# Performance work log

Measured on AMD Instinct MI355X. Metric: run time of the kernel, lower is better.

The kernel has to match this reference:

```python
import jax, jax.numpy as jnp
import numpy as np

N = 10000      # nodes
E = 160000     # edges
B = 16         # graphs in batch
F_NODE = 42
F_EDGE = 12
D = 256        # hidden_dim
H = 4          # heads
C = D // H     # per-head channels = 64
L = 5          # num_layers
NEG_SLOPE = 0.2  # GATConv leaky_relu slope


def layernorm(x, g, b, eps=1e-5):
    mu = jnp.mean(x, axis=-1, keepdims=True)
    var = jnp.var(x, axis=-1, keepdims=True)
    return (x - mu) * jax.lax.rsqrt(var + eps) * g + b


def setup_inputs() -> dict:
    key = jax.random.key(0)
    ks = jax.random.split(key, 20)
    def w(i, shape, scale=0.05):
        return jax.random.normal(ks[i], shape, dtype=jnp.float32) * scale
    return {
        "x": jax.random.normal(ks[0], (N, F_NODE), dtype=jnp.float32),
        "edge_attr": jax.random.normal(ks[1], (E, F_EDGE), dtype=jnp.float32),
        "edge_index": jax.random.randint(ks[2], (2, E), 0, N),
        "batch": jnp.sort(jax.random.randint(ks[3], (N,), 0, B)),
        # node / edge encoders
        "enc_w": w(4, (F_NODE, D)), "enc_b": jnp.zeros((D,), jnp.float32),
        "eenc_w": w(5, (F_EDGE, D)), "eenc_b": jnp.zeros((D,), jnp.float32),
        # stacked GAT layer params [L, ...]
        "gat_w": w(6, (L, D, D)),          # lin_src == lin_dst (shared in PyG for Tensor input)
        "att_src": w(7, (L, H, C)),
        "att_dst": w(8, (L, H, C)),
        "att_edge": w(9, (L, H, C)),
        "gat_ew": w(10, (L, D, D)),        # lin_edge
        "gat_b": jnp.zeros((L, D), jnp.float32),
        "ln_g": jnp.ones((L, D), jnp.float32),
        "ln_b": jnp.zeros((L, D), jnp.float32),
        # attention pooling gate MLP
        "gate_w1": w(11, (D, D)), "gate_b1": jnp.zeros((D,), jnp.float32),
        "gate_w2": w(12, (D, 1)), "gate_b2": jnp.zeros((1,), jnp.float32),
        # MLP readout (mlp_layers=2)
        "ro_w1": w(13, (D, D)), "ro_b1": jnp.zeros((D,), jnp.float32),
        "ro_w2": w(14, (D, D)), "ro_b2": jnp.zeros((D,), jnp.float32),
    }


def reference(x, edge_index, edge_attr, batch, enc_w, enc_b, eenc_w, eenc_b,
              gat_w, att_src, att_dst, att_edge, gat_ew, gat_b, ln_g, ln_b,
              gate_w1, gate_b1, gate_w2, gate_b2, ro_w1, ro_b1, ro_w2, ro_b2):
    src0, dst0 = edge_index[0], edge_index[1]

    # encoders (dropout is identity at eval)
    h = jax.nn.relu(x @ enc_w + enc_b)                      # [N, D]
    e = jax.nn.relu(edge_attr @ eenc_w + eenc_b)            # [E, D]

    # GATConv add_self_loops with fill_value='mean': self-loop edge feature is
    # the mean of incoming edge features per destination node.
    esum = jax.ops.segment_sum(e, dst0, num_segments=N)
    cnt = jax.ops.segment_sum(jnp.ones((E,), e.dtype), dst0, num_segments=N)
    e_self = esum / jnp.maximum(cnt, 1.0)[:, None]
    e_full = jnp.concatenate([e, e_self], axis=0)           # [E+N, D]
    loops = jnp.arange(N)
    src = jnp.concatenate([src0, loops])
    dst = jnp.concatenate([dst0, loops])

    for l in range(L):
        xh = (h @ gat_w[l]).reshape(N, H, C)                # [N, H, C]
        a_s = jnp.einsum('nhc,hc->nh', xh, att_src[l])      # [N, H]
        a_d = jnp.einsum('nhc,hc->nh', xh, att_dst[l])
        eh = (e_full @ gat_ew[l]).reshape(-1, H, C)         # [E+N, H, C]
        a_e = jnp.einsum('ehc,hc->eh', eh, att_edge[l])
        alpha = jax.nn.leaky_relu(a_s[src] + a_d[dst] + a_e, NEG_SLOPE)  # [E+N, H]
        # softmax over incoming edges per destination node (stable)
        m = jax.lax.stop_gradient(jax.ops.segment_max(alpha, dst, num_segments=N))
        ex = jnp.exp(alpha - m[dst])
        den = jax.ops.segment_sum(ex, dst, num_segments=N)
        attn = ex / den[dst]                                # [E+N, H]
        msg = xh[src] * attn[:, :, None]                    # [E+N, H, C]
        out = jax.ops.segment_sum(msg, dst, num_segments=N).reshape(N, D) + gat_b[l]
        out = jax.nn.relu(layernorm(out, ln_g[l], ln_b[l]))
        h = h + out                                         # residual

    # GlobalAttention pooling: softmax(gate_nn(h)) per graph, weighted sum
    gate = (jax.nn.relu(h @ gate_w1 + gate_b1) @ gate_w2 + gate_b2)[:, 0]  # [N]
    gm = jax.lax.stop_gradient(jax.ops.segment_max(gate, batch, num_segments=B))
    ge = jnp.exp(gate - gm[batch])
    gd = jax.ops.segment_sum(ge, batch, num_segments=B)
    wgt = ge / gd[batch]
    g_embed = jax.ops.segment_sum(h * wgt[:, None], batch, num_segments=B)  # [B, D]

    # MLP readout
    return jax.nn.relu(g_embed @ ro_w1 + ro_b1) @ ro_w2 + ro_b2  # [B, D]
```

## Files before the change

### kernel.cpp

```cpp
#include <hip/hip_runtime.h>
#include <math.h>

#define DD 256
#define HH 4
#define CC 64
#define LL 5
#define NEG_SLOPE 0.2f
#define LH 20
#define WCAP 192

typedef __bf16 bf16x8 __attribute__((ext_vector_type(8)));
typedef __bf16 bf16x4 __attribute__((ext_vector_type(4)));
typedef float f32x4 __attribute__((ext_vector_type(4)));

static __device__ __forceinline__ float lrelu(float x) {
    return x > 0.0f ? x : NEG_SLOPE * x;
}

__global__ __launch_bounds__(256) void mega_setup_kernel(
    const float* __restrict__ gat_ew, const float* __restrict__ att_edge,
    float* __restrict__ wproj,
    const float* __restrict__ gat_w, const float* __restrict__ gate_w1,
    __bf16* __restrict__ wf,
    const int* __restrict__ dst_arr, int* __restrict__ deg,
    const float* __restrict__ x, const float* __restrict__ enc_w,
    const float* __restrict__ enc_b, float* __restrict__ h,
    __bf16* __restrict__ hbf,
    float* __restrict__ g_embed, float* __restrict__ gate_out,
    int N, int E, int B) {
    int blk = blockIdx.x;
    int tid = threadIdx.x;
    int EB = (E + 255) >> 8;
    if (blk < 5) {
        int l = blk;
        int k = tid;
        const float* W = gat_ew + (size_t)l * DD * DD;
        const float* att = att_edge + l * DD;
        for (int hh = 0; hh < HH; ++hh) {
            float s = 0.f;
            #pragma unroll
            for (int c = 0; c < CC; ++c)
                s += W[k * DD + hh * CC + c] * att[hh * CC + c];
            wproj[k * LH + l * HH + hh] = s;
        }
        return;
    }
    blk -= 5;
    if (blk < 192) {
        int b = blk;
        int l = b >> 5;
        int rem = b & 31;
        int y = rem >> 3, ks = rem & 7;
        int t = tid >> 6, lane = tid & 63;
        int q = lane >> 4, r15 = lane & 15;
        const float* W = (l < 5) ? (gat_w + (size_t)l * DD * DD) : gate_w1;
        size_t obase = (((size_t)b * 4 + t) * 64 + lane) * 8;
        int kbase = ks * 32 + q * 8;
        int col = y * 64 + t * 16 + r15;
        #pragma unroll
        for (int j = 0; j < 8; ++j)
            wf[obase + j] = (__bf16)W[(size_t)(kbase + j) * DD + col];
        return;
    }
    blk -= 192;
    if (blk < EB) {
        int e = blk * 256 + tid;
        if (e < E) atomicAdd(&deg[dst_arr[e]], 1);
        return;
    }
    blk -= EB;
    if (blk < N) {
        int n = blk;
        __shared__ float xs[42];
        if (tid < 42) xs[tid] = x[(size_t)n * 42 + tid];
        __syncthreads();
        float acc = enc_b[tid];
        #pragma unroll
        for (int f = 0; f < 42; ++f) acc += xs[f] * enc_w[f * DD + tid];
        float v = fmaxf(acc, 0.f);
        h[(size_t)n * DD + tid] = v;
        hbf[(size_t)n * DD + tid] = (__bf16)v;
        return;
    }
    blk -= N;
    if (blk == 0) {
        for (int i = tid; i < B * DD; i += 256) g_embed[i] = 0.f;
        return;
    }
    for (int i = tid; i < N; i += 256) gate_out[i] = 0.f;
}

__global__ __launch_bounds__(1024) void scan_pack_kernel(
    const int* __restrict__ deg, int* __restrict__ row_ptr,
    int* __restrict__ cursor, int n,
    const float* __restrict__ eenc_w, const float* __restrict__ eenc_b,
    const float* __restrict__ wproj, __bf16* __restrict__ wfe,
    __bf16* __restrict__ wfp) {
    int tid = threadIdx.x;
    if (blockIdx.x == 1) {
        {
            int idx = tid;
            int t = idx >> 6, lane = idx & 63;
            int q = lane >> 4, r15 = lane & 15;
            int col = t * 16 + r15;
            #pragma unroll
            for (int j = 0; j < 8; ++j) {
                int k = q * 8 + j;
                float v = (k < 12) ? eenc_w[k * 256 + col]
                                   : (k == 12 ? eenc_b[col] : 0.f);
                wfe[(size_t)idx * 8 + j] = (__bf16)v;
            }
        }
        {
            int idx = tid;
            int sidx = idx >> 6, lane = idx & 63;
            int s = sidx >> 1, t2 = sidx & 1;
            int q = lane >> 4, r15 = lane & 15;
            int col = t2 * 16 + r15;
            #pragma unroll
            for (int j = 0; j < 8; ++j) {
                int k = s * 32 + q * 8 + j;
                float v = (col < LH) ? wproj[k * LH + col] : 0.f;
                wfp[(size_t)idx * 8 + j] = (__bf16)v;
            }
        }
        return;
    }
    __shared__ int wsum[16];
    __shared__ int carry_s;
    int w = tid >> 6, lane = tid & 63;
    if (tid == 0) carry_s = 0;
    __syncthreads();
    for (int base = 0; base < n; base += 1024) {
        int i = base + tid;
        int v = (i < n) ? deg[i] : 0;
        int carry = carry_s;
        int s = v;
        #pragma unroll
        for (int off = 1; off < 64; off <<= 1) {
            int t = __shfl_up(s, off, 64);
            if (lane >= off) s += t;
        }
        if (lane == 63) wsum[w] = s;
        __syncthreads();
        if (w == 0 && lane < 16) {
            int ws = wsum[lane];
            #pragma unroll
            for (int off = 1; off < 16; off <<= 1) {
                int t = __shfl_up(ws, off, 64);
                if (lane >= off) ws += t;
            }
            wsum[lane] = ws;
        }
        __syncthreads();
        int waveoff = (w == 0) ? 0 : wsum[w - 1];
        if (i < n) {
            int ex = carry + waveoff + s - v;
            row_ptr[i] = ex;
            cursor[i] = ex;
        }
        __syncthreads();
        if (tid == 0) carry_s = carry + wsum[15];
        __syncthreads();
    }
    if (tid == 0) row_ptr[n] = carry_s;
}

__global__ void scatter_kernel(const int* __restrict__ src, const int* __restrict__ dst,
                               int* __restrict__ cursor, int* __restrict__ csr_src,
                               int* __restrict__ pos, int E) {
    int e = blockIdx.x * 256 + threadIdx.x;
    if (e >= E) return;
    int d = dst[e];
    int pk = atomicAdd(&cursor[d], 1);
    csr_src[pk] = src[e];
    pos[e] = pk;
}

__global__ __launch_bounds__(256) void edge_mfma_kernel(
    const float* __restrict__ edge_attr, const __bf16* __restrict__ wfe,
    const __bf16* __restrict__ wfp, const int* __restrict__ pos,
    float* __restrict__ a_e_csr, int E) {
    __shared__ __bf16 sm[4][16][264];
    int tid = threadIdx.x;
    int w = tid >> 6, lane = tid & 63;
    int q = lane >> 4, r15 = lane & 15;
    int eb = blockIdx.x * 64 + w * 16;
    int e = eb + r15;
    int ec = min(e, E - 1);
    bf16x8 a1;
    #pragma unroll
    for (int j = 0; j < 8; ++j) a1[j] = (__bf16)0.f;
    if (q == 0) {
        const float4* p = (const float4*)(edge_attr + (size_t)ec * 12);
        float4 p0 = p[0], p1 = p[1];
        a1[0] = (__bf16)p0.x; a1[1] = (__bf16)p0.y; a1[2] = (__bf16)p0.z; a1[3] = (__bf16)p0.w;
        a1[4] = (__bf16)p1.x; a1[5] = (__bf16)p1.y; a1[6] = (__bf16)p1.z; a1[7] = (__bf16)p1.w;
    } else if (q == 1) {
        float4 p2 = *(const float4*)(edge_attr + (size_t)ec * 12 + 8);
        a1[0] = (__bf16)p2.x; a1[1] = (__bf16)p2.y; a1[2] = (__bf16)p2.z; a1[3] = (__bf16)p2.w;
        a1[4] = (__bf16)1.0f;
    }
    const bf16x8* wfeP = (const bf16x8*)wfe;
    f32x4 zero = (f32x4){0.f, 0.f, 0.f, 0.f};
    #pragma unroll
    for (int t = 0; t < 16; ++t) {
        bf16x8 bfr = wfeP[t * 64 + lane];
        f32x4 c = __builtin_amdgcn_mfma_f32_16x16x32_bf16(a1, bfr, zero, 0, 0, 0);
        int col = t * 16 + r15;
        #pragma unroll
        for (int r = 0; r < 4; ++r)
            sm[w][q * 4 + r][col] = (__bf16)fmaxf(c[r], 0.f);
    }
    const bf16x8* wfpP = (const bf16x8*)wfp;
    f32x4 c2[2];
    c2[0] = zero; c2[1] = zero;
    #pragma unroll
    for (int s = 0; s < 8; ++s) {
        bf16x8 a2 = *(const bf16x8*)&sm[w][r15][s * 32 + q * 8];
        #pragma unroll
        for (int t2 = 0; t2 < 2; ++t2)
            c2[t2] = __builtin_amdgcn_mfma_f32_16x16x32_bf16(
                a2, wfpP[(s * 2 + t2) * 64 + lane], c2[t2], 0, 0, 0);
    }
    #pragma unroll
    for (int t2 = 0; t2 < 2; ++t2) {
        int col = t2 * 16 + r15;
        if (col >= LH) continue;
        #pragma unroll
        for (int r = 0; r < 4; ++r) {
            int e2 = eb + q * 4 + r;
            if (e2 < E) {
                int pk = pos[e2];
                a_e_csr[(size_t)pk * LH + col] = c2[t2][r];
            }
        }
    }
}

__global__ void self_ae_kernel(const int* __restrict__ row_ptr,
                               float* __restrict__ a_e_csr, int N, int E) {
    int i = blockIdx.x * 256 + threadIdx.x;
    if (i >= N * LH) return;
    int n = i / LH;
    int j = i % LH;
    int rs = row_ptr[n], re = row_ptr[n + 1];
    float s = 0.f;
    for (int k = rs; k < re; ++k)
        s += a_e_csr[(size_t)k * LH + j];
    a_e_csr[(size_t)(E + n) * LH + j] = s / (float)max(re - rs, 1);
}

__global__ __launch_bounds__(256) void gemm_mfma_kernel(
    const __bf16* __restrict__ hbf, const __bf16* __restrict__ wf,
    __bf16* __restrict__ xhbf, int M,
    const float* __restrict__ att_src, const float* __restrict__ att_dst,
    float* __restrict__ a_s, float* __restrict__ a_d,
    const float* __restrict__ bias, const float* __restrict__ gate_w2,
    const float* __restrict__ gate_b2, float* __restrict__ gate_out) {
    int tid = threadIdx.x;
    int w = tid >> 6, lane = tid & 63;
    int q = lane >> 4, r15 = lane & 15;
    int m0 = blockIdx.x * 64;
    int y2 = blockIdx.y;
    int arow = m0 + w * 16 + r15;
    int arowc = min(arow, M - 1);
    const __bf16* ap = hbf + (size_t)arowc * DD + q * 8;
    const bf16x8* wfP = (const bf16x8*)wf;
    f32x4 acc[8];
    #pragma unroll
    for (int g = 0; g < 8; ++g) acc[g] = (f32x4){0.f, 0.f, 0.f, 0.f};
    #pragma unroll
    for (int ks = 0; ks < 8; ++ks) {
        bf16x8 a = *(const bf16x8*)(ap + ks * 32);
        #pragma unroll
        for (int g = 0; g < 8; ++g) {
            int y = y2 * 2 + (g >> 2);
            int t = g & 3;
            bf16x8 b = wfP[(size_t)(((y * 8 + ks) * 4) + t) * 64 + lane];
            acc[g] = __builtin_amdgcn_mfma_f32_16x16x32_bf16(a, b, acc[g], 0, 0, 0);
        }
    }
    if (xhbf) {
        #pragma unroll
        for (int g = 0; g < 8; ++g) {
            int col = (y2 * 8 + g) * 16 + r15;
            #pragma unroll
            for (int r = 0; r < 4; ++r) {
                int rc = m0 + w * 16 + q * 4 + r;
                if (rc < M) xhbf[(size_t)rc * DD + col] = (__bf16)acc[g][r];
            }
        }
    }
    if (att_src) {
        #pragma unroll
        for (int r = 0; r < 4; ++r) {
            float ps0 = 0.f, pd0 = 0.f, ps1 = 0.f, pd1 = 0.f;
            #pragma unroll
            for (int g = 0; g < 8; ++g) {
                int col = (y2 * 8 + g) * 16 + r15;
                float v = acc[g][r];
                if (g < 4) { ps0 += v * att_src[col]; pd0 += v * att_dst[col]; }
                else       { ps1 += v * att_src[col]; pd1 += v * att_dst[col]; }
            }
            #pragma unroll
            for (int mask = 1; mask < 16; mask <<= 1) {
                ps0 += __shfl_xor(ps0, mask, 64);
                pd0 += __shfl_xor(pd0, mask, 64);
                ps1 += __shfl_xor(ps1, mask, 64);
                pd1 += __shfl_xor(pd1, mask, 64);
            }
            int rc = m0 + w * 16 + q * 4 + r;
            if (r15 == 0 && rc < M) {
                a_s[rc * HH + y2 * 2 + 0] = ps0;
                a_d[rc * HH + y2 * 2 + 0] = pd0;
                a_s[rc * HH + y2 * 2 + 1] = ps1;
                a_d[rc * HH + y2 * 2 + 1] = pd1;
            }
        }
    }
    if (gate_w2) {
        #pragma unroll
        for (int r = 0; r < 4; ++r) {
            float pg = 0.f;
            #pragma unroll
            for (int g = 0; g < 8; ++g) {
                int col = (y2 * 8 + g) * 16 + r15;
                pg += fmaxf(acc[g][r] + bias[col], 0.f) * gate_w2[col];
            }
            #pragma unroll
            for (int mask = 1; mask < 16; mask <<= 1) pg += __shfl_xor(pg, mask, 64);
            int rc = m0 + w * 16 + q * 4 + r;
            if (r15 == 0 && rc < M) {
                float add = pg + (y2 == 0 ? gate_b2[0] : 0.f);
                atomicAdd(&gate_out[rc], add);
            }
        }
    }
}

__global__ __launch_bounds__(256) void gat_message7_kernel(
    const __bf16* __restrict__ xhbf, const float* __restrict__ a_s,
    const float* __restrict__ a_d, const float* __restrict__ a_e,
    const int* __restrict__ row_ptr, const int* __restrict__ csr_src,
    const float* __restrict__ gat_b,
    const float* __restrict__ ln_g, const float* __restrict__ ln_b,
    float* __restrict__ h, __bf16* __restrict__ hbf, int N, int E) {
    __shared__ float lws[4][WCAP * 4];
    __shared__ int lsrc[4][WCAP];
    int tid = threadIdx.x;
    int w = tid >> 6, lane = tid & 63;
    int n = blockIdx.x * 4 + w;
    if (n >= N) return;
    int hh = lane >> 4, j = lane & 15;
    int rs = row_ptr[n], re = row_ptr[n + 1];
    int deg = re - rs;
    float adn = a_d[n * HH + hh];
    float al_self = lrelu(a_s[n * HH + hh] + adn + a_e[(size_t)(E + n) * LH + hh]);
    float m = al_self, den = 0.f;
    for (int k = rs + j; k < re; k += 16) {
        int kk = k - rs;
        int s = csr_src[k];
        float a = lrelu(a_s[s * HH + hh] + adn + a_e[(size_t)k * LH + hh]);
        if (kk < WCAP) {
            lws[w][kk * 4 + hh] = a;
            if (hh == 0) lsrc[w][kk] = s;
        }
        float mn = fmaxf(m, a);
        den = den * __expf(m - mn) + __expf(a - mn);
        m = mn;
    }
    #pragma unroll
    for (int off = 1; off < 16; off <<= 1) {
        float m2 = __shfl_xor(m, off, 64);
        float d2 = __shfl_xor(den, off, 64);
        float mn = fmaxf(m, m2);
        den = den * __expf(m - mn) + d2 * __expf(m2 - mn);
        m = mn;
    }
    den += __expf(al_self - m);
    float inv_den = 1.0f / den;
    int cap = min(deg, WCAP);
    for (int kk = j; kk < cap; kk += 16)
        lws[w][kk * 4 + hh] = __expf(lws[w][kk * 4 + hh] - m) * inv_den;
    float wself = __expf(al_self - m) * inv_den;
    bf16x4 xsb = *((const bf16x4*)(xhbf + (size_t)n * DD) + lane);
    float4 acc;
    acc.x = wself * (float)xsb[0]; acc.y = wself * (float)xsb[1];
    acc.z = wself * (float)xsb[2]; acc.w = wself * (float)xsb[3];
    int k = rs;
    for (; k + 1 < re; k += 2) {
        int kk0 = k - rs, kk1 = kk0 + 1;
        int s0, s1_;
        float w0, w1;
        if (kk1 < WCAP) {
            s0 = lsrc[w][kk0]; s1_ = lsrc[w][kk1];
            w0 = lws[w][kk0 * 4 + hh]; w1 = lws[w][kk1 * 4 + hh];
        } else {
            s0 = csr_src[k]; s1_ = csr_src[k + 1];
            w0 = (kk0 < WCAP) ? lws[w][kk0 * 4 + hh]
               : __expf(lrelu(a_s[s0 * HH + hh] + adn + a_e[(size_t)k * LH + hh]) - m) * inv_den;
            w1 = __expf(lrelu(a_s[s1_ * HH + hh] + adn + a_e[(size_t)(k + 1) * LH + hh]) - m) * inv_den;
        }
        bf16x4 x0 = *((const bf16x4*)(xhbf + (size_t)s0 * DD) + lane);
        bf16x4 x1 = *((const bf16x4*)(xhbf + (size_t)s1_ * DD) + lane);
        acc.x += w0 * (float)x0[0] + w1 * (float)x1[0];
        acc.y += w0 * (float)x0[1] + w1 * (float)x1[1];
        acc.z += w0 * (float)x0[2] + w1 * (float)x1[2];
        acc.w += w0 * (float)x0[3] + w1 * (float)x1[3];
    }
    if (k < re) {
        int kk0 = k - rs;
        int s0;
        float w0;
        if (kk0 < WCAP) { s0 = lsrc[w][kk0]; w0 = lws[w][kk0 * 4 + hh]; }
        else {
            s0 = csr_src[k];
            w0 = __expf(lrelu(a_s[s0 * HH + hh] + adn + a_e[(size_t)k * LH + hh]) - m) * inv_den;
        }
        bf16x4 x0 = *((const bf16x4*)(xhbf + (size_t)s0 * DD) + lane);
        acc.x += w0 * (float)x0[0]; acc.y += w0 * (float)x0[1];
        acc.z += w0 * (float)x0[2]; acc.w += w0 * (float)x0[3];
    }
    float4 gb = *((const float4*)gat_b + lane);
    float4 val;
    val.x = acc.x + gb.x; val.y = acc.y + gb.y;
    val.z = acc.z + gb.z; val.w = acc.w + gb.w;
    float s1 = val.x + val.y + val.z + val.w;
    float s2 = val.x * val.x + val.y * val.y + val.z * val.z + val.w * val.w;
    #pragma unroll
    for (int off = 1; off < 64; off <<= 1) {
        s1 += __shfl_xor(s1, off, 64);
        s2 += __shfl_xor(s2, off, 64);
    }
    float mu = s1 * (1.0f / DD);
    float var = s2 * (1.0f / DD) - mu * mu;
    float rstd = rsqrtf(var + 1e-5f);
    float4 lg = *((const float4*)ln_g + lane);
    float4 lb = *((const float4*)ln_b + lane);
    float4 nv;
    nv.x = fmaxf((val.x - mu) * rstd * lg.x + lb.x, 0.f);
    nv.y = fmaxf((val.y - mu) * rstd * lg.y + lb.y, 0.f);
    nv.z = fmaxf((val.z - mu) * rstd * lg.z + lb.z, 0.f);
    nv.w = fmaxf((val.w - mu) * rstd * lg.w + lb.w, 0.f);
    float4* hp = (float4*)(h + (size_t)n * DD) + lane;
    float4 hv = *hp;
    hv.x += nv.x; hv.y += nv.y; hv.z += nv.z; hv.w += nv.w;
    *hp = hv;
    bf16x4 hb;
    hb[0] = (__bf16)hv.x; hb[1] = (__bf16)hv.y;
    hb[2] = (__bf16)hv.z; hb[3] = (__bf16)hv.w;
    *((bf16x4*)(hbf + (size_t)n * DD) + lane) = hb;
}

__global__ __launch_bounds__(256) void gseg_kernel(
    const float* __restrict__ gate, const int* __restrict__ batch,
    float* __restrict__ gmax, float* __restrict__ gden, int N) {
    int b = blockIdx.x;
    int tid = threadIdx.x;
    __shared__ int bounds[2];
    if (tid < 2) {
        int target = b + tid;
        int lo = 0, hi = N;
        while (lo < hi) {
            int mid = (lo + hi) >> 1;
            if (batch[mid] < target) lo = mid + 1; else hi = mid;
        }
        bounds[tid] = lo;
    }
    __syncthreads();
    int s0 = bounds[0], s1 = bounds[1];
    __shared__ float red[256];
    float m = -1e30f;
    for (int i = s0 + tid; i < s1; i += 256) m = fmaxf(m, gate[i]);
    red[tid] = m;
    __syncthreads();
    for (int off = 128; off; off >>= 1) {
        if (tid < off) red[tid] = fmaxf(red[tid], red[tid + off]);
        __syncthreads();
    }
    float gm = red[0];
    __syncthreads();
    float s = 0.f;
    for (int i = s0 + tid; i < s1; i += 256) s += __expf(gate[i] - gm);
    red[tid] = s;
    __syncthreads();
    for (int off = 128; off; off >>= 1) {
        if (tid < off) red[tid] += red[tid + off];
        __syncthreads();
    }
    if (tid == 0) {
        gmax[b] = gm;
        gden[b] = red[0];
    }
}

#define POOL_CHUNK 32
__global__ __launch_bounds__(256) void pool_scatter_kernel(
    const float* __restrict__ h, const float* __restrict__ gate,
    const float* __restrict__ gmax, const float* __restrict__ gden,
    const int* __restrict__ batch, float* __restrict__ g_embed, int N) {
    int i0 = blockIdx.x * POOL_CHUNK;
    int d = threadIdx.x;
    int iend = min(i0 + POOL_CHUNK, N);
    float acc = 0.f;
    int cur = batch[i0];
    for (int i = i0; i < iend; ++i) {
        int b = batch[i];
        if (b != cur) {
            atomicAdd(&g_embed[cur * DD + d], acc);
            acc = 0.f;
            cur = b;
        }
        float wgt = __expf(gate[i] - gmax[b]) / gden[b];
        acc += wgt * h[(size_t)i * DD + d];
    }
    atomicAdd(&g_embed[cur * DD + d], acc);
}

__global__ __launch_bounds__(256) void readout_kernel(
    const float* __restrict__ g_embed, const float* __restrict__ w1,
    const float* __restrict__ b1, const float* __restrict__ w2,
    const float* __restrict__ b2, float* __restrict__ out) {
    int b = blockIdx.x;
    int tid = threadIdx.x;
    __shared__ float gvec[256];
    __shared__ float hid[256];
    gvec[tid] = g_embed[b * DD + tid];
    __syncthreads();
    float hv = b1[tid];
    for (int k = 0; k < DD; ++k) hv += gvec[k] * w1[k * DD + tid];
    hid[tid] = fmaxf(hv, 0.f);
    __syncthreads();
    float o = b2[tid];
    for (int t = 0; t < DD; ++t) o += hid[t] * w2[t * DD + tid];
    out[b * DD + tid] = o;
}

extern "C" void kernel_launch(void* const* d_in, const int* in_sizes, int n_in,
                              void* d_out, int out_size, void* d_ws, size_t ws_size,
                              hipStream_t stream) {
    const float* x        = (const float*)d_in[0];
    const float* edge_attr= (const float*)d_in[1];
    const int*   edge_idx = (const int*)d_in[2];
    const int*   batch    = (const int*)d_in[3];
    const float* enc_w    = (const float*)d_in[4];
    const float* enc_b    = (const float*)d_in[5];
    const float* eenc_w   = (const float*)d_in[6];
    const float* eenc_b   = (const float*)d_in[7];
    const float* gat_w    = (const float*)d_in[8];
    const float* att_src  = (const float*)d_in[9];
    const float* att_dst  = (const float*)d_in[10];
    const float* att_edge = (const float*)d_in[11];
    const float* gat_ew   = (const float*)d_in[12];
    const float* gat_b    = (const float*)d_in[13];
    const float* ln_g     = (const float*)d_in[14];
    const float* ln_b     = (const float*)d_in[15];
    const float* gate_w1  = (const float*)d_in[16];
    const float* gate_b1  = (const float*)d_in[17];
    const float* gate_w2  = (const float*)d_in[18];
    const float* gate_b2  = (const float*)d_in[19];
    const float* ro_w1    = (const float*)d_in[20];
    const float* ro_b1    = (const float*)d_in[21];
    const float* ro_w2    = (const float*)d_in[22];
    const float* ro_b2    = (const float*)d_in[23];
    float* out = (float*)d_out;

    const int N = in_sizes[0] / 42;
    const int E = in_sizes[1] / 12;
    const int B = out_size / DD;

    char* p = (char*)d_ws;
    auto alloc = [&](size_t bytes) {
        char* r = p;
        p += (bytes + 255) & ~(size_t)255;
        return (void*)r;
    };
    float*  h       = (float*)alloc((size_t)N * DD * 4);
    __bf16* hbf     = (__bf16*)alloc((size_t)N * DD * 2);
    __bf16* xhbf    = (__bf16*)alloc((size_t)N * DD * 2);
    float*  a_s     = (float*)alloc((size_t)N * HH * 4);
    float*  a_d     = (float*)alloc((size_t)N * HH * 4);
    float*  a_e_csr = (float*)alloc((size_t)(E + N) * LH * 4);
    float*  wproj   = (float*)alloc((size_t)DD * LH * 4);
    __bf16* wfe     = (__bf16*)alloc((size_t)16 * 64 * 8 * 2);
    __bf16* wfp     = (__bf16*)alloc((size_t)16 * 64 * 8 * 2);
    __bf16* wf      = (__bf16*)alloc((size_t)6 * DD * DD * 2);
    float*  gate    = (float*)alloc((size_t)N * 4);
    float*  g_embed = (float*)alloc((size_t)B * DD * 4);
    float*  gmax    = (float*)alloc((size_t)B * 4);
    float*  gden    = (float*)alloc((size_t)B * 4);
    int* deg        = (int*)alloc((size_t)N * 4);
    int* row_ptr    = (int*)alloc((size_t)(N + 1) * 4);
    int* cursor     = (int*)alloc((size_t)N * 4);
    int* csr_src    = (int*)alloc((size_t)E * 4);
    int* pos        = (int*)alloc((size_t)E * 4);

    const int* src_arr = edge_idx;
    const int* dst_arr = edge_idx + E;

    hipMemsetAsync(deg, 0, (size_t)N * 4, stream);

    const int EB = (E + 255) / 256;
    int mega_grid = 5 + 192 + EB + N + 2;
    mega_setup_kernel<<<mega_grid, 256, 0, stream>>>(
        gat_ew, att_edge, wproj, gat_w, gate_w1, wf,
        dst_arr, deg, x, enc_w, enc_b, h, hbf, g_embed, gate, N, E, B);
    scan_pack_kernel<<<2, 1024, 0, stream>>>(
        deg, row_ptr, cursor, N, eenc_w, eenc_b, wproj, wfe, wfp);
    scatter_kernel<<<(E + 255) / 256, 256, 0, stream>>>(
        src_arr, dst_arr, cursor, csr_src, pos, E);
    edge_mfma_kernel<<<(E + 63) / 64, 256, 0, stream>>>(
        edge_attr, wfe, wfp, pos, a_e_csr, E);
    self_ae_kernel<<<(N * LH + 255) / 256, 256, 0, stream>>>(
        row_ptr, a_e_csr, N, E);

    dim3 ggrid((N + 63) / 64, 2);
    for (int l = 0; l < LL; ++l) {
        gemm_mfma_kernel<<<ggrid, 256, 0, stream>>>(
            hbf, wf + (size_t)l * DD * DD, xhbf, N,
            att_src + l * DD, att_dst + l * DD, a_s, a_d,
            nullptr, nullptr, nullptr, nullptr);
        gat_message7_kernel<<<(N + 3) / 4, 256, 0, stream>>>(
            xhbf, a_s, a_d, a_e_csr + l * HH, row_ptr, csr_src,
            gat_b + l * DD, ln_g + l * DD, ln_b + l * DD, h, hbf, N, E);
    }

    gemm_mfma_kernel<<<ggrid, 256, 0, stream>>>(
        hbf, wf + (size_t)5 * DD * DD, nullptr, N,
        nullptr, nullptr, nullptr, nullptr,
        gate_b1, gate_w2, gate_b2, gate);
    gseg_kernel<<<B, 256, 0, stream>>>(gate, batch, gmax, gden, N);
    pool_scatter_kernel<<<(N + POOL_CHUNK - 1) / POOL_CHUNK, 256, 0, stream>>>(
        h, gate, gmax, gden, batch, g_embed, N);
    readout_kernel<<<B, 256, 0, stream>>>(g_embed, ro_w1, ro_b1, ro_w2, ro_b2, out);
}
```

Before: 402.6 us.

## Fuse CSR scatter into edge MFMA, split edge attention per layer, unroll gather by four

Removes the separate scatter kernel by doing the atomic cursor slot assignment and csr_src write inside the edge MFMA kernel, keeping slot indices in shared memory instead of a pos array. The edge attention logits move from an interleaved [E+N, 20] layout to per-layer [L][E+N][4] planes, so each message-passing layer reads a contiguous 16-byte row per edge instead of striding over 80 bytes. The message aggregation loop gains a fast path for degree at most WCAP that unrolls the neighbor gather by four, putting more loads in flight. The fusion adds atomics into the MFMA kernel.

```diff
diff --git a/kernel.cpp b/kernel.cpp
--- a/kernel.cpp
+++ b/kernel.cpp
@@ -166,28 +166,26 @@
     if (tid == 0) row_ptr[n] = carry_s;
 }
 
-__global__ void scatter_kernel(const int* __restrict__ src, const int* __restrict__ dst,
-                               int* __restrict__ cursor, int* __restrict__ csr_src,
-                               int* __restrict__ pos, int E) {
-    int e = blockIdx.x * 256 + threadIdx.x;
-    if (e >= E) return;
-    int d = dst[e];
-    int pk = atomicAdd(&cursor[d], 1);
-    csr_src[pk] = src[e];
-    pos[e] = pk;
-}
-
 __global__ __launch_bounds__(256) void edge_mfma_kernel(
     const float* __restrict__ edge_attr, const __bf16* __restrict__ wfe,
-    const __bf16* __restrict__ wfp, const int* __restrict__ pos,
-    float* __restrict__ a_e_csr, int E) {
+    const __bf16* __restrict__ wfp,
+    const int* __restrict__ src_arr, const int* __restrict__ dst_arr,
+    int* __restrict__ cursor, int* __restrict__ csr_src,
+    float* __restrict__ a_e, int E, int N) {
     __shared__ __bf16 sm[4][16][264];
+    __shared__ int pkbuf[4][16];
     int tid = threadIdx.x;
     int w = tid >> 6, lane = tid & 63;
     int q = lane >> 4, r15 = lane & 15;
     int eb = blockIdx.x * 64 + w * 16;
     int e = eb + r15;
     int ec = min(e, E - 1);
+    if (q == 0 && e < E) {
+        int d = dst_arr[e];
+        int pk = atomicAdd(&cursor[d], 1);
+        csr_src[pk] = src_arr[e];
+        pkbuf[w][r15] = pk;
+    }
     bf16x8 a1;
     #pragma unroll
     for (int j = 0; j < 8; ++j) a1[j] = (__bf16)0.f;
@@ -223,32 +221,36 @@
             c2[t2] = __builtin_amdgcn_mfma_f32_16x16x32_bf16(
                 a2, wfpP[(s * 2 + t2) * 64 + lane], c2[t2], 0, 0, 0);
     }
+    size_t stride_l = (size_t)(E + N) * 4;
     #pragma unroll
     for (int t2 = 0; t2 < 2; ++t2) {
         int col = t2 * 16 + r15;
         if (col >= LH) continue;
+        int l = col >> 2, hh = col & 3;
         #pragma unroll
         for (int r = 0; r < 4; ++r) {
             int e2 = eb + q * 4 + r;
             if (e2 < E) {
-                int pk = pos[e2];
-                a_e_csr[(size_t)pk * LH + col] = c2[t2][r];
+                int pk = pkbuf[w][q * 4 + r];
+                a_e[(size_t)l * stride_l + (size_t)pk * 4 + hh] = c2[t2][r];
             }
         }
     }
 }
 
 __global__ void self_ae_kernel(const int* __restrict__ row_ptr,
-                               float* __restrict__ a_e_csr, int N, int E) {
+                               float* __restrict__ a_e, int N, int E) {
     int i = blockIdx.x * 256 + threadIdx.x;
     if (i >= N * LH) return;
     int n = i / LH;
     int j = i % LH;
+    int l = j >> 2, hh = j & 3;
     int rs = row_ptr[n], re = row_ptr[n + 1];
+    size_t base = (size_t)l * (size_t)(E + N) * 4;
     float s = 0.f;
     for (int k = rs; k < re; ++k)
-        s += a_e_csr[(size_t)k * LH + j];
-    a_e_csr[(size_t)(E + n) * LH + j] = s / (float)max(re - rs, 1);
+        s += a_e[base + (size_t)k * 4 + hh];
+    a_e[base + (size_t)(E + n) * 4 + hh] = s / (float)max(re - rs, 1);
 }
 
 __global__ __launch_bounds__(256) void gemm_mfma_kernel(
@@ -339,7 +341,7 @@
     }
 }
 
-__global__ __launch_bounds__(256) void gat_message7_kernel(
+__global__ __launch_bounds__(256) void gat_message8_kernel(
     const __bf16* __restrict__ xhbf, const float* __restrict__ a_s,
     const float* __restrict__ a_d, const float* __restrict__ a_e,
     const int* __restrict__ row_ptr, const int* __restrict__ csr_src,
@@ -356,12 +358,12 @@
     int rs = row_ptr[n], re = row_ptr[n + 1];
     int deg = re - rs;
     float adn = a_d[n * HH + hh];
-    float al_self = lrelu(a_s[n * HH + hh] + adn + a_e[(size_t)(E + n) * LH + hh]);
+    float al_self = lrelu(a_s[n * HH + hh] + adn + a_e[(size_t)(E + n) * 4 + hh]);
     float m = al_self, den = 0.f;
     for (int k = rs + j; k < re; k += 16) {
         int kk = k - rs;
         int s = csr_src[k];
-        float a = lrelu(a_s[s * HH + hh] + adn + a_e[(size_t)k * LH + hh]);
+        float a = lrelu(a_s[s * HH + hh] + adn + a_e[(size_t)k * 4 + hh]);
         if (kk < WCAP) {
             lws[w][kk * 4 + hh] = a;
             if (hh == 0) lsrc[w][kk] = s;
@@ -388,39 +390,45 @@
     float4 acc;
     acc.x = wself * (float)xsb[0]; acc.y = wself * (float)xsb[1];
     acc.z = wself * (float)xsb[2]; acc.w = wself * (float)xsb[3];
-    int k = rs;
-    for (; k + 1 < re; k += 2) {
-        int kk0 = k - rs, kk1 = kk0 + 1;
-        int s0, s1_;
-        float w0, w1;
-        if (kk1 < WCAP) {
-            s0 = lsrc[w][kk0]; s1_ = lsrc[w][kk1];
-            w0 = lws[w][kk0 * 4 + hh]; w1 = lws[w][kk1 * 4 + hh];
-        } else {
-            s0 = csr_src[k]; s1_ = csr_src[k + 1];
-            w0 = (kk0 < WCAP) ? lws[w][kk0 * 4 + hh]
-               : __expf(lrelu(a_s[s0 * HH + hh] + adn + a_e[(size_t)k * LH + hh]) - m) * inv_den;
-            w1 = __expf(lrelu(a_s[s1_ * HH + hh] + adn + a_e[(size_t)(k + 1) * LH + hh]) - m) * inv_den;
-        }
-        bf16x4 x0 = *((const bf16x4*)(xhbf + (size_t)s0 * DD) + lane);
-        bf16x4 x1 = *((const bf16x4*)(xhbf + (size_t)s1_ * DD) + lane);
-        acc.x += w0 * (float)x0[0] + w1 * (float)x1[0];
-        acc.y += w0 * (float)x0[1] + w1 * (float)x1[1];
-        acc.z += w0 * (float)x0[2] + w1 * (float)x1[2];
-        acc.w += w0 * (float)x0[3] + w1 * (float)x1[3];
-    }
-    if (k < re) {
-        int kk0 = k - rs;
-        int s0;
-        float w0;
-        if (kk0 < WCAP) { s0 = lsrc[w][kk0]; w0 = lws[w][kk0 * 4 + hh]; }
-        else {
-            s0 = csr_src[k];
-            w0 = __expf(lrelu(a_s[s0 * HH + hh] + adn + a_e[(size_t)k * LH + hh]) - m) * inv_den;
-        }
-        bf16x4 x0 = *((const bf16x4*)(xhbf + (size_t)s0 * DD) + lane);
-        acc.x += w0 * (float)x0[0]; acc.y += w0 * (float)x0[1];
-        acc.z += w0 * (float)x0[2]; acc.w += w0 * (float)x0[3];
+    if (deg <= WCAP) {
+        int k = rs;
+        for (; k + 3 < re; k += 4) {
+            int kk = k - rs;
+            int s0 = lsrc[w][kk + 0], s1_ = lsrc[w][kk + 1];
+            int s2_ = lsrc[w][kk + 2], s3_ = lsrc[w][kk + 3];
+            float w0 = lws[w][(kk + 0) * 4 + hh], w1 = lws[w][(kk + 1) * 4 + hh];
+            float w2 = lws[w][(kk + 2) * 4 + hh], w3 = lws[w][(kk + 3) * 4 + hh];
+            bf16x4 x0 = *((const bf16x4*)(xhbf + (size_t)s0 * DD) + lane);
+            bf16x4 x1 = *((const bf16x4*)(xhbf + (size_t)s1_ * DD) + lane);
+            bf16x4 x2 = *((const bf16x4*)(xhbf + (size_t)s2_ * DD) + lane);
+            bf16x4 x3 = *((const bf16x4*)(xhbf + (size_t)s3_ * DD) + lane);
+            acc.x += w0 * (float)x0[0] + w1 * (float)x1[0] + w2 * (float)x2[0] + w3 * (float)x3[0];
+            acc.y += w0 * (float)x0[1] + w1 * (float)x1[1] + w2 * (float)x2[1] + w3 * (float)x3[1];
+            acc.z += w0 * (float)x0[2] + w1 * (float)x1[2] + w2 * (float)x2[2] + w3 * (float)x3[2];
+            acc.w += w0 * (float)x0[3] + w1 * (float)x1[3] + w2 * (float)x2[3] + w3 * (float)x3[3];
+        }
+        for (; k < re; ++k) {
+            int kk = k - rs;
+            int s0 = lsrc[w][kk];
+            float w0 = lws[w][kk * 4 + hh];
+            bf16x4 x0 = *((const bf16x4*)(xhbf + (size_t)s0 * DD) + lane);
+            acc.x += w0 * (float)x0[0]; acc.y += w0 * (float)x0[1];
+            acc.z += w0 * (float)x0[2]; acc.w += w0 * (float)x0[3];
+        }
+    } else {
+        for (int k = rs; k < re; ++k) {
+            int kk = k - rs;
+            int s0;
+            float w0;
+            if (kk < WCAP) { s0 = lsrc[w][kk]; w0 = lws[w][kk * 4 + hh]; }
+            else {
+                s0 = csr_src[k];
+                w0 = __expf(lrelu(a_s[s0 * HH + hh] + adn + a_e[(size_t)k * 4 + hh]) - m) * inv_den;
+            }
+            bf16x4 x0 = *((const bf16x4*)(xhbf + (size_t)s0 * DD) + lane);
+            acc.x += w0 * (float)x0[0]; acc.y += w0 * (float)x0[1];
+            acc.z += w0 * (float)x0[2]; acc.w += w0 * (float)x0[3];
+        }
     }
     float4 gb = *((const float4*)gat_b + lane);
     float4 val;
@@ -581,7 +589,7 @@
     __bf16* xhbf    = (__bf16*)alloc((size_t)N * DD * 2);
     float*  a_s     = (float*)alloc((size_t)N * HH * 4);
     float*  a_d     = (float*)alloc((size_t)N * HH * 4);
-    float*  a_e_csr = (float*)alloc((size_t)(E + N) * LH * 4);
+    float*  a_e_csr = (float*)alloc((size_t)LL * (E + N) * 4 * 4);
     float*  wproj   = (float*)alloc((size_t)DD * LH * 4);
     __bf16* wfe     = (__bf16*)alloc((size_t)16 * 64 * 8 * 2);
     __bf16* wfp     = (__bf16*)alloc((size_t)16 * 64 * 8 * 2);
@@ -594,7 +602,6 @@
     int* row_ptr    = (int*)alloc((size_t)(N + 1) * 4);
     int* cursor     = (int*)alloc((size_t)N * 4);
     int* csr_src    = (int*)alloc((size_t)E * 4);
-    int* pos        = (int*)alloc((size_t)E * 4);
 
     const int* src_arr = edge_idx;
     const int* dst_arr = edge_idx + E;
@@ -608,21 +615,20 @@
         dst_arr, deg, x, enc_w, enc_b, h, hbf, g_embed, gate, N, E, B);
     scan_pack_kernel<<<2, 1024, 0, stream>>>(
         deg, row_ptr, cursor, N, eenc_w, eenc_b, wproj, wfe, wfp);
-    scatter_kernel<<<(E + 255) / 256, 256, 0, stream>>>(
-        src_arr, dst_arr, cursor, csr_src, pos, E);
     edge_mfma_kernel<<<(E + 63) / 64, 256, 0, stream>>>(
-        edge_attr, wfe, wfp, pos, a_e_csr, E);
+        edge_attr, wfe, wfp, src_arr, dst_arr, cursor, csr_src, a_e_csr, E, N);
     self_ae_kernel<<<(N * LH + 255) / 256, 256, 0, stream>>>(
         row_ptr, a_e_csr, N, E);
 
     dim3 ggrid((N + 63) / 64, 2);
+    size_t lstride = (size_t)(E + N) * 4;
     for (int l = 0; l < LL; ++l) {
         gemm_mfma_kernel<<<ggrid, 256, 0, stream>>>(
             hbf, wf + (size_t)l * DD * DD, xhbf, N,
             att_src + l * DD, att_dst + l * DD, a_s, a_d,
             nullptr, nullptr, nullptr, nullptr);
-        gat_message7_kernel<<<(N + 3) / 4, 256, 0, stream>>>(
-            xhbf, a_s, a_d, a_e_csr + l * HH, row_ptr, csr_src,
+        gat_message8_kernel<<<(N + 3) / 4, 256, 0, stream>>>(
+            xhbf, a_s, a_d, a_e_csr + (size_t)l * lstride, row_ptr, csr_src,
             gat_b + l * DD, ln_g + l * DD, ln_b + l * DD, h, hbf, N, E);
     }
 
```

Result: faster. 376.4 us, median of 2 (-6.5%).
